# Kernel tuning notes

Hardware: AMD Instinct MI355X
Metric: run time of the kernel (lower is better)

## Reference

```python
import jax, jax.numpy as jnp
import numpy as np

B, N, C = 4, 4096, 256
H, D, K = 8, 32, 16  # heads, dim_head, knn


def setup_inputs() -> dict:
    key = jax.random.key(0)
    ks = jax.random.split(key, 7)
    s = 1.0 / np.sqrt(C)
    return {
        "x": jax.random.normal(ks[0], (B, N, C), dtype=jnp.float32),
        "Wq": jax.random.normal(ks[1], (C, H * D), dtype=jnp.float32) * s,
        "bq": jnp.zeros((H * D,), dtype=jnp.float32),
        "Wk": jax.random.normal(ks[2], (C, H * D), dtype=jnp.float32) * s,
        "bk": jnp.zeros((H * D,), dtype=jnp.float32),
        "Wv": jax.random.normal(ks[3], (C, H * D), dtype=jnp.float32) * s,
        "bv": jnp.zeros((H * D,), dtype=jnp.float32),
    }


def _knn_indices(x):
    # squared euclidean distances per batch: [B, N, N]
    sq = jnp.sum(x * x, axis=-1)
    d2 = sq[:, :, None] + sq[:, None, :] - 2.0 * jnp.einsum("bnc,bmc->bnm", x, x)
    # exclude self-loops (loop=False)
    eye = jnp.eye(x.shape[1], dtype=bool)
    d2 = jnp.where(eye[None], jnp.inf, d2)
    # k nearest neighbors (smallest distance)
    _, idx = jax.lax.top_k(-d2, K)  # [B, N, K]
    return idx


def reference(x, Wq, bq, Wk, bk, Wv, bv):
    idx = _knn_indices(x)  # [B, N, K] neighbor (source) node ids per target node
    # gather neighbor features: [B, N, K, C]
    xj = jax.vmap(lambda xb, ib: xb[ib])(x, idx)
    q = (x @ Wq + bq).reshape(B, N, H, D)           # target-node queries
    ke = (xj @ Wk + bk).reshape(B, N, K, H, D)      # per-edge keys
    ve = (xj @ Wv + bv).reshape(B, N, K, H, D)      # per-edge values
    scale = 1.0 / np.sqrt(D)
    scores = jnp.einsum("bnhd,bnkhd->bnkh", q, ke) * scale
    alpha = jax.nn.softmax(scores, axis=2)          # softmax over each node's K neighbors
    out = jnp.einsum("bnkh,bnkhd->bnhd", alpha, ve)
    return out.reshape(B, N, H * D)
```

## Files before the change

kernel.cpp:

```cpp
#include <hip/hip_runtime.h>
#include <cstdint>
#include <cstddef>

#define N_ 4096
#define C_ 256

typedef _Float16 h8 __attribute__((ext_vector_type(8)));
typedef _Float16 h4 __attribute__((ext_vector_type(4)));
typedef float f4 __attribute__((ext_vector_type(4)));

__device__ __forceinline__ void gl2lds16(const void* g, void* l) {
  __builtin_amdgcn_global_load_lds((const __attribute__((address_space(1))) void*)g,
                                   (__attribute__((address_space(3))) void*)l, 16, 0, 0);
}

__global__ __launch_bounds__(256) void k_prep(const float* __restrict__ x,
                                              float* __restrict__ sq,
                                              _Float16* __restrict__ xh,
                                              _Float16* __restrict__ xl) {
  int wave = threadIdx.x >> 6, lane = threadIdx.x & 63;
  int row = blockIdx.x * 4 + wave;
  size_t off = (size_t)row * C_ + lane * 4;
  float4 v = *(const float4*)(x + off);
  h4 hi; hi[0] = (_Float16)v.x; hi[1] = (_Float16)v.y;
         hi[2] = (_Float16)v.z; hi[3] = (_Float16)v.w;
  h4 lo; lo[0] = (_Float16)(v.x - (float)hi[0]); lo[1] = (_Float16)(v.y - (float)hi[1]);
         lo[2] = (_Float16)(v.z - (float)hi[2]); lo[3] = (_Float16)(v.w - (float)hi[3]);
  *(h4*)(xh + off) = hi;
  *(h4*)(xl + off) = lo;
  float s = v.x * v.x + v.y * v.y + v.z * v.z + v.w * v.w;
  s += __shfl_xor(s, 32); s += __shfl_xor(s, 16); s += __shfl_xor(s, 8);
  s += __shfl_xor(s, 4);  s += __shfl_xor(s, 2);  s += __shfl_xor(s, 1);
  if (lane == 0) sq[row] = s;
}

__global__ __launch_bounds__(256) void k_wsplit(const float* __restrict__ Wq,
                                                const float* __restrict__ Wk,
                                                const float* __restrict__ Wv,
                                                _Float16* __restrict__ wh,
                                                _Float16* __restrict__ wl) {
  int g = blockIdx.x * 256 + threadIdx.x;
  int m = g >> 16, e = g & 65535;
  int k = e >> 8, j = e & 255;
  const float* W = (m == 0) ? Wq : ((m == 1) ? Wk : Wv);
  float v = W[k * 256 + j];
  _Float16 hi = (_Float16)v;
  _Float16 lo = (_Float16)(v - (float)hi);
  wh[m * 65536 + j * 256 + k] = hi;
  wl[m * 65536 + j * 256 + k] = lo;
}

__global__ __launch_bounds__(256, 2) void k_proj(const _Float16* __restrict__ xh,
                                                 const _Float16* __restrict__ xl,
                                                 const _Float16* __restrict__ wh,
                                                 const _Float16* __restrict__ wl,
                                                 const float* __restrict__ bqp,
                                                 const float* __restrict__ bkp,
                                                 const float* __restrict__ bvp,
                                                 float* __restrict__ qf,
                                                 float* __restrict__ kf,
                                                 float* __restrict__ vf) {
  int tid = threadIdx.x;
  int m  = blockIdx.x / 128;
  int rb = blockIdx.x % 128;
  int wave = tid >> 6, lane = tid & 63, quad = lane >> 4, l16 = lane & 15;
  const float* bb = (m == 0) ? bqp : ((m == 1) ? bkp : bvp);
  float* dst      = (m == 0) ? qf  : ((m == 1) ? kf  : vf);
  int row0 = rb * 128 + wave * 32;

  h8 Ah[2][8], Al[2][8];
#pragma unroll
  for (int rt = 0; rt < 2; rt++)
#pragma unroll
    for (int kc = 0; kc < 8; kc++) {
      size_t off = (size_t)(row0 + rt * 16 + l16) * C_ + kc * 32 + quad * 8;
      Ah[rt][kc] = *(const h8*)(xh + off);
      Al[rt][kc] = *(const h8*)(xl + off);
    }
  const _Float16* whm = wh + (size_t)m * 65536;
  const _Float16* wlm = wl + (size_t)m * 65536;

#pragma unroll 1
  for (int cp = 0; cp < 2; cp++) {
    f4 acc[2][8];
#pragma unroll
    for (int rt = 0; rt < 2; rt++)
#pragma unroll
      for (int ct = 0; ct < 8; ct++) acc[rt][ct] = f4{0.f, 0.f, 0.f, 0.f};
#pragma unroll
    for (int kc = 0; kc < 8; kc++) {
#pragma unroll
      for (int ct = 0; ct < 8; ct++) {
        int col = cp * 128 + ct * 16 + l16;
        h8 bh = *(const h8*)(whm + (size_t)col * 256 + kc * 32 + quad * 8);
        h8 bl = *(const h8*)(wlm + (size_t)col * 256 + kc * 32 + quad * 8);
#pragma unroll
        for (int rt = 0; rt < 2; rt++) {
          acc[rt][ct] = __builtin_amdgcn_mfma_f32_16x16x32_f16(Ah[rt][kc], bh, acc[rt][ct], 0, 0, 0);
          acc[rt][ct] = __builtin_amdgcn_mfma_f32_16x16x32_f16(Ah[rt][kc], bl, acc[rt][ct], 0, 0, 0);
          acc[rt][ct] = __builtin_amdgcn_mfma_f32_16x16x32_f16(Al[rt][kc], bh, acc[rt][ct], 0, 0, 0);
        }
      }
    }
#pragma unroll
    for (int rt = 0; rt < 2; rt++)
#pragma unroll
      for (int ct = 0; ct < 8; ct++) {
        int col = cp * 128 + ct * 16 + l16;
        float bias = bb[col];
#pragma unroll
        for (int i = 0; i < 4; i++) {
          int r = row0 + rt * 16 + quad * 4 + i;
          dst[(size_t)r * C_ + col] = acc[rt][ct][i] + bias;
        }
      }
  }
}

__global__ __launch_bounds__(256, 2) void k_knn(const _Float16* __restrict__ xh,
                                                const _Float16* __restrict__ xl,
                                                const float* __restrict__ sq,
                                                double* __restrict__ pd) {
  __shared__ __align__(16) _Float16 Bh[16 * 528];
  __shared__ __align__(16) _Float16 Bl[16 * 528];
  __shared__ __align__(16) float sc[128 * 36];
  __shared__ float sqS[32];

  int tid = threadIdx.x;
  int wave = tid >> 6, lane = tid & 63, quad = lane >> 4, l16 = lane & 15;
  int bid = blockIdx.x;
  int s4 = bid & 3, tile = (bid >> 2) & 31, b = bid >> 7;
  int bN = b * N_, n0 = tile * 128, src0g = s4 * 1024;

  h8 Ah[2][8], Al[2][8];
  int tb = bN + n0 + wave * 32;
#pragma unroll
  for (int rt = 0; rt < 2; rt++)
#pragma unroll
    for (int kc = 0; kc < 8; kc++) {
      size_t off = (size_t)(tb + rt * 16 + l16) * C_ + kc * 32 + quad * 8;
      Ah[rt][kc] = *(const h8*)(xh + off);
      Al[rt][kc] = *(const h8*)(xl + off);
    }
  float sqT[2][4];
#pragma unroll
  for (int rt = 0; rt < 2; rt++)
#pragma unroll
    for (int i = 0; i < 4; i++)
      sqT[rt][i] = sq[tb + rt * 16 + quad * 4 + i];

  double karr[16];
#pragma unroll
  for (int p = 0; p < 16; p++) karr[p] = 1e300;
  int rowo = tid & 127, half = tid >> 7;

  {
    const _Float16* gh = xh + (size_t)(bN + src0g) * C_ + lane * 8;
    const _Float16* gl = xl + (size_t)(bN + src0g) * C_ + lane * 8;
#pragma unroll
    for (int k = 0; k < 4; k++) {
      int seg = wave * 4 + k;
      gl2lds16(gh + seg * 512, &Bh[seg * 528]);
      gl2lds16(gl + seg * 512, &Bl[seg * 528]);
    }
    if (tid < 32) sqS[tid] = sq[bN + src0g + tid];
  }

  int hb0 = ((l16 >> 1) * 528) + ((l16 & 1) * 256) + quad * 8;
  int hb1 = (((16 + l16) >> 1) * 528) + ((l16 & 1) * 256) + quad * 8;

#pragma unroll 1
  for (int ch = 0; ch < 32; ch++) {
    int src0 = src0g + ch * 32;
    __syncthreads();

    f4 acc[2][2];
#pragma unroll
    for (int rt = 0; rt < 2; rt++)
#pragma unroll
      for (int ct = 0; ct < 2; ct++) acc[rt][ct] = f4{0.f, 0.f, 0.f, 0.f};
#pragma unroll
    for (int kc = 0; kc < 8; kc++) {
      h8 bh0 = *(const h8*)(&Bh[hb0 + kc * 32]);
      h8 bh1 = *(const h8*)(&Bh[hb1 + kc * 32]);
      h8 bl0 = *(const h8*)(&Bl[hb0 + kc * 32]);
      h8 bl1 = *(const h8*)(&Bl[hb1 + kc * 32]);
#pragma unroll
      for (int rt = 0; rt < 2; rt++) {
        acc[rt][0] = __builtin_amdgcn_mfma_f32_16x16x32_f16(Ah[rt][kc], bh0, acc[rt][0], 0, 0, 0);
        acc[rt][0] = __builtin_amdgcn_mfma_f32_16x16x32_f16(Ah[rt][kc], bl0, acc[rt][0], 0, 0, 0);
        acc[rt][0] = __builtin_amdgcn_mfma_f32_16x16x32_f16(Al[rt][kc], bh0, acc[rt][0], 0, 0, 0);
        acc[rt][1] = __builtin_amdgcn_mfma_f32_16x16x32_f16(Ah[rt][kc], bh1, acc[rt][1], 0, 0, 0);
        acc[rt][1] = __builtin_amdgcn_mfma_f32_16x16x32_f16(Ah[rt][kc], bl1, acc[rt][1], 0, 0, 0);
        acc[rt][1] = __builtin_amdgcn_mfma_f32_16x16x32_f16(Al[rt][kc], bh1, acc[rt][1], 0, 0, 0);
      }
    }
    float sqSr[2] = {sqS[l16], sqS[16 + l16]};
#pragma unroll
    for (int rt = 0; rt < 2; rt++)
#pragma unroll
      for (int ct = 0; ct < 2; ct++) {
        int c = ct * 16 + l16;
#pragma unroll
        for (int i = 0; i < 4; i++) {
          int r = wave * 32 + rt * 16 + quad * 4 + i;
          float d2 = sqT[rt][i] + sqSr[ct] - 2.0f * acc[rt][ct][i];
          if (n0 + r == src0 + c) d2 = 1e38f;
          sc[r * 36 + c] = d2;
        }
      }
    __syncthreads();

    if (ch < 31) {
      int srcn = src0 + 32;
      const _Float16* gh = xh + (size_t)(bN + srcn) * C_ + lane * 8;
      const _Float16* gl = xl + (size_t)(bN + srcn) * C_ + lane * 8;
#pragma unroll
      for (int k = 0; k < 4; k++) {
        int seg = wave * 4 + k;
        gl2lds16(gh + seg * 512, &Bh[seg * 528]);
        gl2lds16(gl + seg * 512, &Bl[seg * 528]);
      }
      if (tid < 32) sqS[tid] = sq[bN + srcn + tid];
    }

    float dv[16];
#pragma unroll
    for (int k4 = 0; k4 < 4; k4++)
      *(float4*)&dv[k4 * 4] = *(const float4*)(&sc[rowo * 36 + half * 16 + k4 * 4]);
#pragma unroll
    for (int j = 0; j < 16; j++) {
      double key = (double)dv[j];
      key = __longlong_as_double(__double_as_longlong(key) |
                                 (unsigned)(src0 + half * 16 + j));
      if (key < karr[15]) {
#pragma unroll
        for (int p = 15; p >= 1; p--)
          karr[p] = fmin(fmax(key, karr[p - 1]), karr[p]);
        karr[0] = fmin(karr[0], key);
      }
    }
  }

  __syncthreads();
  double* scd = (double*)sc;
  if (tid >= 128) {
#pragma unroll
    for (int p = 0; p < 16; p++) scd[(tid - 128) * 17 + p] = karr[p];
  }
  __syncthreads();
  if (tid < 128) {
#pragma unroll
    for (int j = 0; j < 16; j++) {
      double key = scd[tid * 17 + j];
      if (key < karr[15]) {
#pragma unroll
        for (int p = 15; p >= 1; p--)
          karr[p] = fmin(fmax(key, karr[p - 1]), karr[p]);
        karr[0] = fmin(karr[0], key);
      }
    }
#pragma unroll
    for (int p = 0; p < 16; p++)
      pd[((size_t)bid * 128 + tid) * 16 + p] = karr[p];
  }
}

__global__ __launch_bounds__(256) void k_kmerge(const double* __restrict__ pd,
                                                int* __restrict__ idxo) {
  int g = blockIdx.x * 256 + threadIdx.x;
  int b = g >> 12, n = g & 4095;
  int tile = n >> 7, r = n & 127;
  size_t base[4]; int p[4]; double hd[4];
#pragma unroll
  for (int s = 0; s < 4; s++) {
    base[s] = (size_t)(((b * 32 + tile) * 4 + s) * 128 + r) * 16;
    p[s] = 0;
    hd[s] = pd[base[s]];
  }
#pragma unroll
  for (int k = 0; k < 16; k++) {
    int bs = 0; double bd = hd[0];
#pragma unroll
    for (int s = 1; s < 4; s++) if (hd[s] < bd) { bd = hd[s]; bs = s; }
    idxo[(size_t)g * 16 + k] = (int)(__double_as_longlong(bd) & 0xFFF);
    p[bs]++;
    hd[bs] = (p[bs] < 16) ? pd[base[bs] + p[bs]] : 1e301;
  }
}

__global__ __launch_bounds__(256) void k_attn(const float* __restrict__ qf,
                                              const float* __restrict__ kf,
                                              const float* __restrict__ vf,
                                              const int* __restrict__ idxv,
                                              float* __restrict__ out) {
  int wave = threadIdx.x >> 6, lane = threadIdx.x & 63;
  int g = blockIdx.x * 4 + wave;
  int bN = (g >> 12) << 12;
  float4 q4 = *(const float4*)(qf + (size_t)g * C_ + lane * 4);
  int my = idxv[(size_t)g * 16 + (lane & 15)];
  const float scale = 0.17677669529663687f;

  float s[16];
  float4 vv[16];
#pragma unroll
  for (int j = 0; j < 16; j++) {
    int nb = __shfl(my, j);
    size_t base = (size_t)(bN + nb) * C_ + lane * 4;
    float4 k4 = *(const float4*)(kf + base);
    vv[j] = *(const float4*)(vf + base);
    float p = k4.x * q4.x + k4.y * q4.y + k4.z * q4.z + k4.w * q4.w;
    p += __shfl_xor(p, 1); p += __shfl_xor(p, 2); p += __shfl_xor(p, 4);
    s[j] = p * scale;
  }
  float mx = s[0];
#pragma unroll
  for (int j = 1; j < 16; j++) mx = fmaxf(mx, s[j]);
  float den = 0.f;
#pragma unroll
  for (int j = 0; j < 16; j++) { s[j] = __expf(s[j] - mx); den += s[j]; }
  float inv = 1.0f / den;
  float4 o; o.x = 0.f; o.y = 0.f; o.z = 0.f; o.w = 0.f;
#pragma unroll
  for (int j = 0; j < 16; j++) {
    float w = s[j] * inv;
    o.x = fmaf(w, vv[j].x, o.x); o.y = fmaf(w, vv[j].y, o.y);
    o.z = fmaf(w, vv[j].z, o.z); o.w = fmaf(w, vv[j].w, o.w);
  }
  *(float4*)(out + (size_t)g * C_ + lane * 4) = o;
}

extern "C" void kernel_launch(void* const* d_in, const int* in_sizes, int n_in,
                              void* d_out, int out_size, void* d_ws, size_t ws_size,
                              hipStream_t stream) {
  const float* x  = (const float*)d_in[0];
  const float* Wq = (const float*)d_in[1];
  const float* bq = (const float*)d_in[2];
  const float* Wk = (const float*)d_in[3];
  const float* bk = (const float*)d_in[4];
  const float* Wv = (const float*)d_in[5];
  const float* bv = (const float*)d_in[6];
  float* out = (float*)d_out;

  char* ws = (char*)d_ws;
  float*     sqp  = (float*)(ws + 0);
  _Float16*  xh   = (_Float16*)(ws + 65536);
  _Float16*  xl   = (_Float16*)(ws + 8454144);
  float*     qf   = (float*)(ws + 16842752);
  float*     kf   = (float*)(ws + 33619968);
  float*     vf   = (float*)(ws + 50397184);
  double*    pd   = (double*)(ws + 67174400);
  int*       idxb = (int*)  (ws + 75563008);
  _Float16*  whf  = (_Float16*)(ws + 76611584);
  _Float16*  wlf  = (_Float16*)(ws + 77004800);

  k_prep  <<<4096, 256, 0, stream>>>(x, sqp, xh, xl);
  k_wsplit<<<768,  256, 0, stream>>>(Wq, Wk, Wv, whf, wlf);
  k_proj  <<<384,  256, 0, stream>>>(xh, xl, whf, wlf, bq, bk, bv, qf, kf, vf);
  k_knn   <<<512,  256, 0, stream>>>(xh, xl, sqp, pd);
  k_kmerge<<<64,   256, 0, stream>>>(pd, idxb);
  k_attn  <<<4096, 256, 0, stream>>>(qf, kf, vf, idxb, out);
}
```

Measured before the change: 348.9 us.

## Threshold-filter kNN candidates into LDS buffer and store K/V in fp16

Replaces the per-thread insertion of every distance into a 16-entry sorted register list with a threshold filter. Candidates below the current 16th-best distance are appended to a small per-row LDS buffer via atomics, and 128 threads merge them into the sorted list, with overflow handled by iterating and retightening the threshold. The goal is to avoid most of the compare-and-insert work once the threshold has tightened. Separately, the key and value projections are stored as fp16 to halve the gather traffic in the attention kernel, at some cost in precision. The filter adds extra barriers per chunk and changes the way work is split between threads.

```diff
diff --git a/kernel.cpp b/kernel.cpp
--- a/kernel.cpp
+++ b/kernel.cpp
@@ -4,6 +4,7 @@
 
 #define N_ 4096
 #define C_ 256
+#define QD 8
 
 typedef _Float16 h8 __attribute__((ext_vector_type(8)));
 typedef _Float16 h4 __attribute__((ext_vector_type(4)));
@@ -58,14 +59,13 @@
                                                  const float* __restrict__ bkp,
                                                  const float* __restrict__ bvp,
                                                  float* __restrict__ qf,
-                                                 float* __restrict__ kf,
-                                                 float* __restrict__ vf) {
+                                                 _Float16* __restrict__ kfh,
+                                                 _Float16* __restrict__ vfh) {
   int tid = threadIdx.x;
   int m  = blockIdx.x / 128;
   int rb = blockIdx.x % 128;
   int wave = tid >> 6, lane = tid & 63, quad = lane >> 4, l16 = lane & 15;
   const float* bb = (m == 0) ? bqp : ((m == 1) ? bkp : bvp);
-  float* dst      = (m == 0) ? qf  : ((m == 1) ? kf  : vf);
   int row0 = rb * 128 + wave * 32;
 
   h8 Ah[2][8], Al[2][8];
@@ -111,7 +111,10 @@
 #pragma unroll
         for (int i = 0; i < 4; i++) {
           int r = row0 + rt * 16 + quad * 4 + i;
-          dst[(size_t)r * C_ + col] = acc[rt][ct][i] + bias;
+          float v = acc[rt][ct][i] + bias;
+          if (m == 0)      qf[(size_t)r * C_ + col] = v;
+          else if (m == 1) kfh[(size_t)r * C_ + col] = (_Float16)v;
+          else             vfh[(size_t)r * C_ + col] = (_Float16)v;
         }
       }
   }
@@ -124,13 +127,21 @@
   __shared__ __align__(16) _Float16 Bh[16 * 528];
   __shared__ __align__(16) _Float16 Bl[16 * 528];
   __shared__ __align__(16) float sc[128 * 36];
+  __shared__ __align__(16) double buf[128 * QD];
+  __shared__ float tauS[128];
+  __shared__ unsigned cntS[128];
   __shared__ float sqS[32];
-
+  __shared__ int ovf;
+
+  const float INF = __builtin_inff();
   int tid = threadIdx.x;
   int wave = tid >> 6, lane = tid & 63, quad = lane >> 4, l16 = lane & 15;
   int bid = blockIdx.x;
   int s4 = bid & 3, tile = (bid >> 2) & 31, b = bid >> 7;
   int bN = b * N_, n0 = tile * 128, src0g = s4 * 1024;
+
+  if (tid < 128) { tauS[tid] = 1e37f; cntS[tid] = 0u; }
+  if (tid == 0) ovf = 0;
 
   h8 Ah[2][8], Al[2][8];
   int tb = bN + n0 + wave * 32;
@@ -205,7 +216,7 @@
         for (int i = 0; i < 4; i++) {
           int r = wave * 32 + rt * 16 + quad * 4 + i;
           float d2 = sqT[rt][i] + sqSr[ct] - 2.0f * acc[rt][ct][i];
-          if (n0 + r == src0 + c) d2 = 1e38f;
+          if (n0 + r == src0 + c) d2 = INF;
           sc[r * 36 + c] = d2;
         }
       }
@@ -224,35 +235,59 @@
       if (tid < 32) sqS[tid] = sq[bN + srcn + tid];
     }
 
-    float dv[16];
-#pragma unroll
-    for (int k4 = 0; k4 < 4; k4++)
-      *(float4*)&dv[k4 * 4] = *(const float4*)(&sc[rowo * 36 + half * 16 + k4 * 4]);
-#pragma unroll
-    for (int j = 0; j < 16; j++) {
-      double key = (double)dv[j];
-      key = __longlong_as_double(__double_as_longlong(key) |
-                                 (unsigned)(src0 + half * 16 + j));
-      if (key < karr[15]) {
-#pragma unroll
-        for (int p = 15; p >= 1; p--)
-          karr[p] = fmin(fmax(key, karr[p - 1]), karr[p]);
-        karr[0] = fmin(karr[0], key);
-      }
-    }
-  }
-
-  __syncthreads();
-  double* scd = (double*)sc;
-  if (tid >= 128) {
-#pragma unroll
-    for (int p = 0; p < 16; p++) scd[(tid - 128) * 17 + p] = karr[p];
-  }
-  __syncthreads();
+    float tau = tauS[rowo];
+#pragma unroll 1
+    for (int iter = 0; iter < 8; iter++) {
+#pragma unroll
+      for (int k4 = 0; k4 < 4; k4++) {
+        float4 d4 = *(const float4*)(&sc[rowo * 36 + half * 16 + k4 * 4]);
+        float dvv[4];
+        *(float4*)dvv = d4;
+#pragma unroll
+        for (int e = 0; e < 4; e++) {
+          if (dvv[e] <= tau) {
+            unsigned pos = atomicAdd(&cntS[rowo], 1u);
+            if (pos < (unsigned)QD) {
+              int c = half * 16 + k4 * 4 + e;
+              double key = (double)dvv[e];
+              key = __longlong_as_double(__double_as_longlong(key) |
+                                         (unsigned)(src0 + c));
+              buf[rowo * QD + pos] = key;
+              sc[rowo * 36 + c] = INF;
+            } else {
+              ovf = 1;
+            }
+          }
+        }
+      }
+      __syncthreads();
+      int need = ovf;
+      __syncthreads();
+      if (!need) break;
+      if (tid == 0) ovf = 0;
+      if (tid < 128) {
+        unsigned c = cntS[tid]; if (c > (unsigned)QD) c = (unsigned)QD;
+        for (unsigned j = 0; j < c; j++) {
+          double key = buf[tid * QD + j];
+          if (key < karr[15]) {
+#pragma unroll
+            for (int p = 15; p >= 1; p--)
+              karr[p] = fmin(fmax(key, karr[p - 1]), karr[p]);
+            karr[0] = fmin(karr[0], key);
+          }
+        }
+        cntS[tid] = 0u;
+        tauS[tid] = fminf((float)karr[15], 1e37f);
+      }
+      __syncthreads();
+      tau = tauS[rowo];
+    }
+  }
+
   if (tid < 128) {
-#pragma unroll
-    for (int j = 0; j < 16; j++) {
-      double key = scd[tid * 17 + j];
+    unsigned c = cntS[tid]; if (c > (unsigned)QD) c = (unsigned)QD;
+    for (unsigned j = 0; j < c; j++) {
+      double key = buf[tid * QD + j];
       if (key < karr[15]) {
 #pragma unroll
         for (int p = 15; p >= 1; p--)
@@ -290,8 +325,8 @@
 }
 
 __global__ __launch_bounds__(256) void k_attn(const float* __restrict__ qf,
-                                              const float* __restrict__ kf,
-                                              const float* __restrict__ vf,
+                                              const _Float16* __restrict__ kf,
+                                              const _Float16* __restrict__ vf,
                                               const int* __restrict__ idxv,
                                               float* __restrict__ out) {
   int wave = threadIdx.x >> 6, lane = threadIdx.x & 63;
@@ -302,14 +337,15 @@
   const float scale = 0.17677669529663687f;
 
   float s[16];
-  float4 vv[16];
+  h4 vv[16];
 #pragma unroll
   for (int j = 0; j < 16; j++) {
     int nb = __shfl(my, j);
     size_t base = (size_t)(bN + nb) * C_ + lane * 4;
-    float4 k4 = *(const float4*)(kf + base);
-    vv[j] = *(const float4*)(vf + base);
-    float p = k4.x * q4.x + k4.y * q4.y + k4.z * q4.z + k4.w * q4.w;
+    h4 k4 = *(const h4*)(kf + base);
+    vv[j] = *(const h4*)(vf + base);
+    float p = (float)k4[0] * q4.x + (float)k4[1] * q4.y +
+              (float)k4[2] * q4.z + (float)k4[3] * q4.w;
     p += __shfl_xor(p, 1); p += __shfl_xor(p, 2); p += __shfl_xor(p, 4);
     s[j] = p * scale;
   }
@@ -324,8 +360,8 @@
 #pragma unroll
   for (int j = 0; j < 16; j++) {
     float w = s[j] * inv;
-    o.x = fmaf(w, vv[j].x, o.x); o.y = fmaf(w, vv[j].y, o.y);
-    o.z = fmaf(w, vv[j].z, o.z); o.w = fmaf(w, vv[j].w, o.w);
+    o.x = fmaf(w, (float)vv[j][0], o.x); o.y = fmaf(w, (float)vv[j][1], o.y);
+    o.z = fmaf(w, (float)vv[j][2], o.z); o.w = fmaf(w, (float)vv[j][3], o.w);
   }
   *(float4*)(out + (size_t)g * C_ + lane * 4) = o;
 }
@@ -347,17 +383,17 @@
   _Float16*  xh   = (_Float16*)(ws + 65536);
   _Float16*  xl   = (_Float16*)(ws + 8454144);
   float*     qf   = (float*)(ws + 16842752);
-  float*     kf   = (float*)(ws + 33619968);
-  float*     vf   = (float*)(ws + 50397184);
-  double*    pd   = (double*)(ws + 67174400);
-  int*       idxb = (int*)  (ws + 75563008);
-  _Float16*  whf  = (_Float16*)(ws + 76611584);
-  _Float16*  wlf  = (_Float16*)(ws + 77004800);
+  _Float16*  kfh  = (_Float16*)(ws + 33619968);
+  _Float16*  vfh  = (_Float16*)(ws + 42008576);
+  double*    pd   = (double*)(ws + 50397184);
+  int*       idxb = (int*)  (ws + 58785792);
+  _Float16*  whf  = (_Float16*)(ws + 59834368);
+  _Float16*  wlf  = (_Float16*)(ws + 60227584);
 
   k_prep  <<<4096, 256, 0, stream>>>(x, sqp, xh, xl);
   k_wsplit<<<768,  256, 0, stream>>>(Wq, Wk, Wv, whf, wlf);
-  k_proj  <<<384,  256, 0, stream>>>(xh, xl, whf, wlf, bq, bk, bv, qf, kf, vf);
+  k_proj  <<<384,  256, 0, stream>>>(xh, xl, whf, wlf, bq, bk, bv, qf, kfh, vfh);
   k_knn   <<<512,  256, 0, stream>>>(xh, xl, sqp, pd);
   k_kmerge<<<64,   256, 0, stream>>>(pd, idxb);
-  k_attn  <<<4096, 256, 0, stream>>>(qf, kf, vf, idxb, out);
-}
+  k_attn  <<<4096, 256, 0, stream>>>(qf, kfh, vfh, idxb, out);
+}
```

Measured after the change: 373.1 us. +7.0%, slower.
